# Optimization experiments

Hardware: AMD Instinct MI355X
Metric: run time of the kernel (lower is better)

The kernel has to match this reference:

```python
import jax, jax.numpy as jnp
import numpy as np

T, B, D, H = 2048, 64, 256, 512

def setup_inputs() -> dict:
    key = jax.random.key(0)
    ks = jax.random.split(key, 4)
    s = 1.0 / np.sqrt(D + H)  # nn.Linear default uniform scale approximated with normal*s
    return {
        "x": jax.random.normal(ks[0], (T, B, D), dtype=jnp.float32),
        "h0": jnp.zeros((B, H), dtype=jnp.float32),
        "Wz": jax.random.normal(ks[1], (D + H, H), dtype=jnp.float32) * s,
        "bz": jnp.zeros((H,), dtype=jnp.float32),
        "Wr": jax.random.normal(ks[2], (D + H, H), dtype=jnp.float32) * s,
        "br": jnp.zeros((H,), dtype=jnp.float32),
        "Wh": jax.random.normal(ks[3], (D + H, H), dtype=jnp.float32) * s,
        "bh": jnp.zeros((H,), dtype=jnp.float32),
    }

def reference(x, h0, Wz, bz, Wr, br, Wh, bh):
    """GRU over time: x [T,B,D], h0 [B,H]; returns hidden history [T,B,H]."""
    def step(h, xt):
        xh = jnp.concatenate([xt, h], axis=-1)          # [B, D+H]
        z = jax.nn.sigmoid(xh @ Wz + bz)                # update gate
        r = jax.nn.sigmoid(xh @ Wr + br)                # reset gate
        xrh = jnp.concatenate([xt, r * h], axis=-1)     # [B, D+H]
        h_tilde = jnp.tanh(xrh @ Wh + bh)               # candidate state
        h_new = (1.0 - z) * h + z * h_tilde
        return h_new, h_new
    _, hist = jax.lax.scan(step, h0, x)
    return hist
```

## Files before the change

### kernel.cpp

```cpp
#include <hip/hip_runtime.h>
#include <stdint.h>


#define T_STEPS 2048
#define B_SZ    64
#define D_SZ    256
#define H_SZ    512
#define NGROUP  4
#define NWG     64
#define MB      16
#define CPW     6

typedef __attribute__((ext_vector_type(8))) short  short8;
typedef __attribute__((ext_vector_type(4))) float  f32x4;

__device__ __forceinline__ unsigned short f2bf(float v) {
  uint32_t u = __float_as_uint(v);
  return (unsigned short)((u + 0x7fffu + ((u >> 16) & 1u)) >> 16);
}
__device__ __forceinline__ float bf2f(unsigned short h) {
  return __uint_as_float(((uint32_t)h) << 16);
}
__device__ __forceinline__ void splitf(float v, short& hi, short& lo) {
  unsigned short h = f2bf(v);
  hi = (short)h;
  lo = (short)f2bf(v - bf2f(h));
}
__device__ __forceinline__ uint32_t packf(float v) {
  unsigned short h = f2bf(v);
  unsigned short l = f2bf(v - bf2f(h));
  return ((uint32_t)h << 16) | (uint32_t)l;
}
__device__ __forceinline__ float unpackf(uint32_t p) {
  return __uint_as_float(p & 0xffff0000u) + __uint_as_float(p << 16);
}

__device__ __forceinline__ uint32_t aload32(const uint32_t* p) {
  return __hip_atomic_load(p, __ATOMIC_RELAXED, __HIP_MEMORY_SCOPE_AGENT);
}
__device__ __forceinline__ unsigned long long aload64(const uint32_t* p) {
  return __hip_atomic_load((const unsigned long long*)p, __ATOMIC_RELAXED,
                           __HIP_MEMORY_SCOPE_AGENT);
}
__device__ __forceinline__ void astore32(uint32_t* p, uint32_t v) {
  __hip_atomic_store(p, v, __ATOMIC_RELAXED, __HIP_MEMORY_SCOPE_AGENT);
}

__device__ __forceinline__ void poll_flags(const uint32_t* fl, uint32_t tgt,
                                           int lane, int& cap) {
  int guard = 0;
  for (;;) {
    uint32_t v = aload32(fl + lane);
    if (__all((int)(v >= tgt))) break;
    if (++guard > cap) { cap = 256; break; }
    __builtin_amdgcn_s_sleep(1);
  }
}

__global__ void __launch_bounds__(256, 1)
gru_persistent(const float* __restrict__ x, const float* __restrict__ h0,
               const float* __restrict__ Wz, const float* __restrict__ bz,
               const float* __restrict__ Wr, const float* __restrict__ br,
               const float* __restrict__ Wh, const float* __restrict__ bh,
               float* __restrict__ out,
               uint32_t* zr_flg, uint32_t* h_flg,
               uint32_t* h_pk, uint32_t* rh_pk, uint32_t* z_pk)
{
  __shared__ float partT[16 * 64];
  __shared__ float bias1s[16];
  __shared__ float bias2s[8];

  const int tid  = threadIdx.x;
  const int wv   = tid >> 6;
  const int lane = tid & 63;
  const int blk  = blockIdx.x;
  const int g    = blk >> 6;
  const int wid  = blk & 63;
  const int m0   = g * MB;
  const bool isZ = (wid < 32);
  const int c1   = (wid & 31) * 16;
  const int c2   = wid * 8;
  const float* W1 = isZ ? Wz : Wr;

  const int n     = lane & 15;
  const int kq    = lane >> 4;
  const int bfrag = m0 + n;
  const int m2    = kq * 4 + wv;
  const int n2    = n;
  const int b2    = m0 + m2;

  uint32_t* my_zr = zr_flg + g * 64;
  uint32_t* my_h  = h_flg  + g * 64;

  short8 w1h[CPW], w1l[CPW], w2h[CPW], w2l[CPW];
  #pragma unroll
  for (int i = 0; i < CPW; ++i) {
    const int ch = wv * CPW + i;
    #pragma unroll
    for (int j = 0; j < 8; ++j) {
      const int k = ch * 32 + kq * 8 + j;
      short hi, lo;
      splitf(W1[(size_t)k * H_SZ + c1 + n], hi, lo);
      w1h[i][j] = hi; w1l[i][j] = lo;
      float v = (n < 8) ? Wh[(size_t)k * H_SZ + c2 + n] : 0.f;
      splitf(v, hi, lo);
      w2h[i][j] = hi; w2l[i][j] = lo;
    }
  }
  if (tid < 16)      bias1s[tid] = isZ ? bz[c1 + tid] : br[c1 + tid];
  else if (tid < 24) bias2s[tid - 16] = bh[c2 + (tid - 16)];
  __syncthreads();

  float hreg = (n2 < 8) ? h0[(size_t)b2 * H_SZ + c2 + n2] : 0.f;

  int cap = 1 << 20;

  #pragma unroll 1
  for (int t = 0; t < T_STEPS; ++t) {
    short8 ah[CPW], al[CPW];

    #pragma unroll
    for (int i = 0; i < CPW; ++i) {
      const int ch = wv * CPW + i;
      if (ch < 8) {
        const float* xp = x + ((size_t)t * B_SZ + bfrag) * D_SZ + ch * 32 + kq * 8;
        float4 f0 = *(const float4*)xp;
        float4 f1 = *(const float4*)(xp + 4);
        float f[8] = {f0.x, f0.y, f0.z, f0.w, f1.x, f1.y, f1.z, f1.w};
        #pragma unroll
        for (int j = 0; j < 8; ++j) { short hi, lo; splitf(f[j], hi, lo); ah[i][j] = hi; al[i][j] = lo; }
      }
    }

    if (t > 0) poll_flags(my_h, (uint32_t)t, lane, cap);

    uint32_t hpu = 0; float hp0 = 0.f;
    if (!isZ) {
      if (t > 0) hpu = aload32(h_pk + (size_t)b2 * H_SZ + c1 + n2);
      else       hp0 = h0[(size_t)b2 * H_SZ + c1 + n2];
    }

    #pragma unroll
    for (int i = 0; i < CPW; ++i) {
      const int ch = wv * CPW + i;
      if (ch >= 8) {
        const int kh = ch * 32 - 256 + kq * 8;
        if (t > 0) {
          const uint32_t* hp = h_pk + (size_t)bfrag * H_SZ + kh;
          unsigned long long q0 = aload64(hp),     q1 = aload64(hp + 2);
          unsigned long long q2 = aload64(hp + 4), q3 = aload64(hp + 6);
          uint32_t u[8] = {(uint32_t)q0, (uint32_t)(q0 >> 32), (uint32_t)q1, (uint32_t)(q1 >> 32),
                           (uint32_t)q2, (uint32_t)(q2 >> 32), (uint32_t)q3, (uint32_t)(q3 >> 32)};
          #pragma unroll
          for (int j = 0; j < 8; ++j) { ah[i][j] = (short)(u[j] >> 16); al[i][j] = (short)(u[j] & 0xffffu); }
        } else {
          const float* hp = h0 + (size_t)bfrag * H_SZ + kh;
          float4 f0 = *(const float4*)hp;
          float4 f1 = *(const float4*)(hp + 4);
          float f[8] = {f0.x, f0.y, f0.z, f0.w, f1.x, f1.y, f1.z, f1.w};
          #pragma unroll
          for (int j = 0; j < 8; ++j) { short hi, lo; splitf(f[j], hi, lo); ah[i][j] = hi; al[i][j] = lo; }
        }
      }
    }

    {
      f32x4 acc = {0.f, 0.f, 0.f, 0.f};
      #pragma unroll
      for (int i = 0; i < CPW; ++i) {
        acc = __builtin_amdgcn_mfma_f32_16x16x32_bf16(ah[i], w1h[i], acc, 0, 0, 0);
        acc = __builtin_amdgcn_mfma_f32_16x16x32_bf16(al[i], w1h[i], acc, 0, 0, 0);
        acc = __builtin_amdgcn_mfma_f32_16x16x32_bf16(ah[i], w1l[i], acc, 0, 0, 0);
      }
      #pragma unroll
      for (int r = 0; r < 4; ++r) partT[(wv * 4 + r) * 64 + lane] = acc[r];
    }
    __syncthreads();

    {
      float s = partT[(0 + wv) * 64 + lane] + partT[(4 + wv) * 64 + lane]
              + partT[(8 + wv) * 64 + lane] + partT[(12 + wv) * 64 + lane] + bias1s[n2];
      float sg = 1.f / (1.f + __expf(-s));
      if (isZ) {
        astore32(z_pk + (size_t)b2 * H_SZ + c1 + n2, __float_as_uint(sg));
      } else {
        float hp = (t > 0) ? unpackf(hpu) : hp0;
        astore32(rh_pk + (size_t)b2 * H_SZ + c1 + n2, packf(sg * hp));
      }
    }
    asm volatile("s_waitcnt vmcnt(0)" ::: "memory");
    __syncthreads();
    if (tid == 0) astore32(my_zr + wid, (uint32_t)(t + 1));

    poll_flags(my_zr, (uint32_t)(t + 1), lane, cap);

    uint32_t zu = 0;
    if (n2 < 8) zu = aload32(z_pk + (size_t)b2 * H_SZ + c2 + n2);

    #pragma unroll
    for (int i = 0; i < CPW; ++i) {
      const int ch = wv * CPW + i;
      if (ch >= 8) {
        const int kh = ch * 32 - 256 + kq * 8;
        const uint32_t* rp = rh_pk + (size_t)bfrag * H_SZ + kh;
        unsigned long long q0 = aload64(rp),     q1 = aload64(rp + 2);
        unsigned long long q2 = aload64(rp + 4), q3 = aload64(rp + 6);
        uint32_t u[8] = {(uint32_t)q0, (uint32_t)(q0 >> 32), (uint32_t)q1, (uint32_t)(q1 >> 32),
                         (uint32_t)q2, (uint32_t)(q2 >> 32), (uint32_t)q3, (uint32_t)(q3 >> 32)};
        #pragma unroll
        for (int j = 0; j < 8; ++j) { ah[i][j] = (short)(u[j] >> 16); al[i][j] = (short)(u[j] & 0xffffu); }
      }
    }

    {
      f32x4 acc = {0.f, 0.f, 0.f, 0.f};
      #pragma unroll
      for (int i = 0; i < CPW; ++i) {
        acc = __builtin_amdgcn_mfma_f32_16x16x32_bf16(ah[i], w2h[i], acc, 0, 0, 0);
        acc = __builtin_amdgcn_mfma_f32_16x16x32_bf16(al[i], w2h[i], acc, 0, 0, 0);
        acc = __builtin_amdgcn_mfma_f32_16x16x32_bf16(ah[i], w2l[i], acc, 0, 0, 0);
      }
      #pragma unroll
      for (int r = 0; r < 4; ++r) partT[(wv * 4 + r) * 64 + lane] = acc[r];
    }
    __syncthreads();

    float hn = 0.f; bool live = (n2 < 8);
    if (live) {
      float s = partT[(0 + wv) * 64 + lane] + partT[(4 + wv) * 64 + lane]
              + partT[(8 + wv) * 64 + lane] + partT[(12 + wv) * 64 + lane] + bias2s[n2];
      float e  = __expf(2.f * s);
      float ht = 1.f - 2.f / (e + 1.f);
      float zf = __uint_as_float(zu);
      hn = (1.f - zf) * hreg + zf * ht;
      hreg = hn;
      astore32(h_pk + (size_t)b2 * H_SZ + c2 + n2, packf(hn));
    }
    asm volatile("s_waitcnt vmcnt(0)" ::: "memory");
    __syncthreads();
    if (tid == 0) astore32(my_h + wid, (uint32_t)(t + 1));

    if (live)
      __builtin_nontemporal_store(hn, out + ((size_t)t * B_SZ + b2) * H_SZ + c2 + n2);
  }
}

extern "C" void kernel_launch(void* const* d_in, const int* in_sizes, int n_in,
                              void* d_out, int out_size, void* d_ws, size_t ws_size,
                              hipStream_t stream) {
  const float* x  = (const float*)d_in[0];
  const float* h0 = (const float*)d_in[1];
  const float* Wz = (const float*)d_in[2];
  const float* bz = (const float*)d_in[3];
  const float* Wr = (const float*)d_in[4];
  const float* br = (const float*)d_in[5];
  const float* Wh = (const float*)d_in[6];
  const float* bh = (const float*)d_in[7];
  float* out = (float*)d_out;

  char* ws = (char*)d_ws;
  uint32_t* zr_flg = (uint32_t*)(ws + 0);
  uint32_t* h_flg  = (uint32_t*)(ws + 16384);
  uint32_t* h_pk   = (uint32_t*)(ws + 32768);
  uint32_t* rh_pk  = (uint32_t*)(ws + 163840);
  uint32_t* z_pk   = (uint32_t*)(ws + 294912);

  hipMemsetAsync(d_ws, 0, 32768, stream);
  gru_persistent<<<dim3(NGROUP * NWG), dim3(256), 0, stream>>>(
      x, h0, Wz, bz, Wr, br, Wh, bh, out,
      zr_flg, h_flg, h_pk, rh_pk, z_pk);
}
```

Before: 25.18 ms.

## Replace flag barriers with step-tagged 64-bit data words and a single epoch flag

Each shared value (h, r*h, z) is now stored as a 64-bit word whose upper half holds the step number. Consumers poll the data itself until every tag reaches the target step, which removes the separate flag-store and flag-poll round trips and the vmcnt drains. A single epoch counter per workgroup guards against overwriting h before all peers have read it (write-after-read), and the full __syncthreads calls become s_barrier after an LDS wait. The cost is twice the global traffic per exchanged value, all of it through per-element 64-bit atomic loads, plus a memset of a larger workspace.

```diff
diff --git a/kernel.cpp b/kernel.cpp
--- a/kernel.cpp
+++ b/kernel.cpp
@@ -13,6 +13,7 @@
 
 typedef __attribute__((ext_vector_type(8))) short  short8;
 typedef __attribute__((ext_vector_type(4))) float  f32x4;
+typedef unsigned long long u64;
 
 __device__ __forceinline__ unsigned short f2bf(float v) {
   uint32_t u = __float_as_uint(v);
@@ -38,23 +39,19 @@
 __device__ __forceinline__ uint32_t aload32(const uint32_t* p) {
   return __hip_atomic_load(p, __ATOMIC_RELAXED, __HIP_MEMORY_SCOPE_AGENT);
 }
-__device__ __forceinline__ unsigned long long aload64(const uint32_t* p) {
-  return __hip_atomic_load((const unsigned long long*)p, __ATOMIC_RELAXED,
-                           __HIP_MEMORY_SCOPE_AGENT);
-}
 __device__ __forceinline__ void astore32(uint32_t* p, uint32_t v) {
   __hip_atomic_store(p, v, __ATOMIC_RELAXED, __HIP_MEMORY_SCOPE_AGENT);
 }
-
-__device__ __forceinline__ void poll_flags(const uint32_t* fl, uint32_t tgt,
-                                           int lane, int& cap) {
-  int guard = 0;
-  for (;;) {
-    uint32_t v = aload32(fl + lane);
-    if (__all((int)(v >= tgt))) break;
-    if (++guard > cap) { cap = 256; break; }
-    __builtin_amdgcn_s_sleep(1);
-  }
+__device__ __forceinline__ u64 aload64p(const u64* p) {
+  return __hip_atomic_load(p, __ATOMIC_RELAXED, __HIP_MEMORY_SCOPE_AGENT);
+}
+__device__ __forceinline__ void astore64(u64* p, u64 v) {
+  __hip_atomic_store(p, v, __ATOMIC_RELAXED, __HIP_MEMORY_SCOPE_AGENT);
+}
+
+__device__ __forceinline__ void lds_barrier() {
+  asm volatile("s_waitcnt lgkmcnt(0)" ::: "memory");
+  __builtin_amdgcn_s_barrier();
 }
 
 __global__ void __launch_bounds__(256, 1)
@@ -63,8 +60,8 @@
                const float* __restrict__ Wr, const float* __restrict__ br,
                const float* __restrict__ Wh, const float* __restrict__ bh,
                float* __restrict__ out,
-               uint32_t* zr_flg, uint32_t* h_flg,
-               uint32_t* h_pk, uint32_t* rh_pk, uint32_t* z_pk)
+               uint32_t* epoch,
+               u64* h_pk, u64* rh_pk, u64* z_pk)
 {
   __shared__ float partT[16 * 64];
   __shared__ float bias1s[16];
@@ -89,8 +86,7 @@
   const int n2    = n;
   const int b2    = m0 + m2;
 
-  uint32_t* my_zr = zr_flg + g * 64;
-  uint32_t* my_h  = h_flg  + g * 64;
+  uint32_t* my_ep = epoch + g * 64;
 
   short8 w1h[CPW], w1l[CPW], w2h[CPW], w2l[CPW];
   #pragma unroll
@@ -132,28 +128,43 @@
       }
     }
 
-    if (t > 0) poll_flags(my_h, (uint32_t)t, lane, cap);
-
-    uint32_t hpu = 0; float hp0 = 0.f;
-    if (!isZ) {
-      if (t > 0) hpu = aload32(h_pk + (size_t)b2 * H_SZ + c1 + n2);
-      else       hp0 = h0[(size_t)b2 * H_SZ + c1 + n2];
-    }
-
-    #pragma unroll
-    for (int i = 0; i < CPW; ++i) {
-      const int ch = wv * CPW + i;
-      if (ch >= 8) {
-        const int kh = ch * 32 - 256 + kq * 8;
-        if (t > 0) {
-          const uint32_t* hp = h_pk + (size_t)bfrag * H_SZ + kh;
-          unsigned long long q0 = aload64(hp),     q1 = aload64(hp + 2);
-          unsigned long long q2 = aload64(hp + 4), q3 = aload64(hp + 6);
-          uint32_t u[8] = {(uint32_t)q0, (uint32_t)(q0 >> 32), (uint32_t)q1, (uint32_t)(q1 >> 32),
-                           (uint32_t)q2, (uint32_t)(q2 >> 32), (uint32_t)q3, (uint32_t)(q3 >> 32)};
-          #pragma unroll
-          for (int j = 0; j < 8; ++j) { ah[i][j] = (short)(u[j] >> 16); al[i][j] = (short)(u[j] & 0xffffu); }
-        } else {
+    uint32_t hpv = 0; float hp0 = 0.f;
+    if (t > 0) {
+      const uint32_t tgt = (uint32_t)t;
+      int guard = 0;
+      for (;;) {
+        uint32_t mt = 0xffffffffu;
+        if (!isZ) {
+          u64 q = aload64p(h_pk + (size_t)b2 * H_SZ + c1 + n2);
+          hpv = (uint32_t)q;
+          uint32_t tg = (uint32_t)(q >> 32); mt = tg < mt ? tg : mt;
+        }
+        #pragma unroll
+        for (int i = 0; i < CPW; ++i) {
+          const int ch = wv * CPW + i;
+          if (ch >= 8) {
+            const int kh = ch * 32 - 256 + kq * 8;
+            const u64* hp = h_pk + (size_t)bfrag * H_SZ + kh;
+            #pragma unroll
+            for (int j = 0; j < 8; ++j) {
+              u64 q = aload64p(hp + j);
+              uint32_t tg = (uint32_t)(q >> 32); mt = tg < mt ? tg : mt;
+              uint32_t v = (uint32_t)q;
+              ah[i][j] = (short)(v >> 16); al[i][j] = (short)(v & 0xffffu);
+            }
+          }
+        }
+        if (__all((int)(mt >= tgt))) break;
+        if (++guard > cap) { cap = 256; break; }
+        __builtin_amdgcn_s_sleep(1);
+      }
+    } else {
+      if (!isZ) hp0 = h0[(size_t)b2 * H_SZ + c1 + n2];
+      #pragma unroll
+      for (int i = 0; i < CPW; ++i) {
+        const int ch = wv * CPW + i;
+        if (ch >= 8) {
+          const int kh = ch * 32 - 256 + kq * 8;
           const float* hp = h0 + (size_t)bfrag * H_SZ + kh;
           float4 f0 = *(const float4*)hp;
           float4 f1 = *(const float4*)(hp + 4);
@@ -175,42 +186,57 @@
       #pragma unroll
       for (int r = 0; r < 4; ++r) partT[(wv * 4 + r) * 64 + lane] = acc[r];
     }
-    __syncthreads();
+    lds_barrier();
+
+    if (tid == 0) astore32(my_ep + wid, (uint32_t)(t + 1));
 
     {
       float s = partT[(0 + wv) * 64 + lane] + partT[(4 + wv) * 64 + lane]
               + partT[(8 + wv) * 64 + lane] + partT[(12 + wv) * 64 + lane] + bias1s[n2];
       float sg = 1.f / (1.f + __expf(-s));
+      const u64 tagw = ((u64)(uint32_t)(t + 1)) << 32;
       if (isZ) {
-        astore32(z_pk + (size_t)b2 * H_SZ + c1 + n2, __float_as_uint(sg));
+        astore64(z_pk + (size_t)b2 * H_SZ + c1 + n2, tagw | (u64)__float_as_uint(sg));
       } else {
-        float hp = (t > 0) ? unpackf(hpu) : hp0;
-        astore32(rh_pk + (size_t)b2 * H_SZ + c1 + n2, packf(sg * hp));
-      }
-    }
-    asm volatile("s_waitcnt vmcnt(0)" ::: "memory");
-    __syncthreads();
-    if (tid == 0) astore32(my_zr + wid, (uint32_t)(t + 1));
-
-    poll_flags(my_zr, (uint32_t)(t + 1), lane, cap);
+        float hp = (t > 0) ? unpackf(hpv) : hp0;
+        astore64(rh_pk + (size_t)b2 * H_SZ + c1 + n2, tagw | (u64)packf(sg * hp));
+      }
+    }
+    lds_barrier();
 
     uint32_t zu = 0;
-    if (n2 < 8) zu = aload32(z_pk + (size_t)b2 * H_SZ + c2 + n2);
-
-    #pragma unroll
-    for (int i = 0; i < CPW; ++i) {
-      const int ch = wv * CPW + i;
-      if (ch >= 8) {
-        const int kh = ch * 32 - 256 + kq * 8;
-        const uint32_t* rp = rh_pk + (size_t)bfrag * H_SZ + kh;
-        unsigned long long q0 = aload64(rp),     q1 = aload64(rp + 2);
-        unsigned long long q2 = aload64(rp + 4), q3 = aload64(rp + 6);
-        uint32_t u[8] = {(uint32_t)q0, (uint32_t)(q0 >> 32), (uint32_t)q1, (uint32_t)(q1 >> 32),
-                         (uint32_t)q2, (uint32_t)(q2 >> 32), (uint32_t)q3, (uint32_t)(q3 >> 32)};
+    {
+      const uint32_t tgt2 = (uint32_t)(t + 1);
+      int guard = 0;
+      for (;;) {
+        uint32_t mt = 0xffffffffu;
+        u64 zq = 0;
+        if (n2 < 8) {
+          zq = aload64p(z_pk + (size_t)b2 * H_SZ + c2 + n2);
+          uint32_t tg = (uint32_t)(zq >> 32); mt = tg < mt ? tg : mt;
+        }
         #pragma unroll
-        for (int j = 0; j < 8; ++j) { ah[i][j] = (short)(u[j] >> 16); al[i][j] = (short)(u[j] & 0xffffu); }
-      }
-    }
+        for (int i = 0; i < CPW; ++i) {
+          const int ch = wv * CPW + i;
+          if (ch >= 8) {
+            const int kh = ch * 32 - 256 + kq * 8;
+            const u64* rp = rh_pk + (size_t)bfrag * H_SZ + kh;
+            #pragma unroll
+            for (int j = 0; j < 8; ++j) {
+              u64 q = aload64p(rp + j);
+              uint32_t tg = (uint32_t)(q >> 32); mt = tg < mt ? tg : mt;
+              uint32_t v = (uint32_t)q;
+              ah[i][j] = (short)(v >> 16); al[i][j] = (short)(v & 0xffffu);
+            }
+          }
+        }
+        if (__all((int)(mt >= tgt2))) { zu = (uint32_t)zq; break; }
+        if (++guard > cap) { cap = 256; zu = (uint32_t)zq; break; }
+        __builtin_amdgcn_s_sleep(1);
+      }
+    }
+
+    uint32_t ep = aload32(my_ep + lane);
 
     {
       f32x4 acc = {0.f, 0.f, 0.f, 0.f};
@@ -223,9 +249,9 @@
       #pragma unroll
       for (int r = 0; r < 4; ++r) partT[(wv * 4 + r) * 64 + lane] = acc[r];
     }
-    __syncthreads();
-
-    float hn = 0.f; bool live = (n2 < 8);
+    lds_barrier();
+
+    float hn = 0.f; const bool live = (n2 < 8);
     if (live) {
       float s = partT[(0 + wv) * 64 + lane] + partT[(4 + wv) * 64 + lane]
               + partT[(8 + wv) * 64 + lane] + partT[(12 + wv) * 64 + lane] + bias2s[n2];
@@ -234,14 +260,23 @@
       float zf = __uint_as_float(zu);
       hn = (1.f - zf) * hreg + zf * ht;
       hreg = hn;
-      astore32(h_pk + (size_t)b2 * H_SZ + c2 + n2, packf(hn));
-    }
-    asm volatile("s_waitcnt vmcnt(0)" ::: "memory");
-    __syncthreads();
-    if (tid == 0) astore32(my_h + wid, (uint32_t)(t + 1));
-
-    if (live)
+    }
+
+    {
+      int guard = 0;
+      while (!__all((int)(ep >= (uint32_t)(t + 1)))) {
+        if (++guard > cap) { cap = 256; break; }
+        __builtin_amdgcn_s_sleep(1);
+        ep = aload32(my_ep + lane);
+      }
+    }
+
+    if (live) {
+      const u64 tagw = ((u64)(uint32_t)(t + 1)) << 32;
+      astore64(h_pk + (size_t)b2 * H_SZ + c2 + n2, tagw | (u64)packf(hn));
       __builtin_nontemporal_store(hn, out + ((size_t)t * B_SZ + b2) * H_SZ + c2 + n2);
+    }
+    lds_barrier();
   }
 }
 
@@ -259,14 +294,13 @@
   float* out = (float*)d_out;
 
   char* ws = (char*)d_ws;
-  uint32_t* zr_flg = (uint32_t*)(ws + 0);
-  uint32_t* h_flg  = (uint32_t*)(ws + 16384);
-  uint32_t* h_pk   = (uint32_t*)(ws + 32768);
-  uint32_t* rh_pk  = (uint32_t*)(ws + 163840);
-  uint32_t* z_pk   = (uint32_t*)(ws + 294912);
-
-  hipMemsetAsync(d_ws, 0, 32768, stream);
+  uint32_t* epoch = (uint32_t*)(ws + 0);
+  u64* h_pk  = (u64*)(ws + 4096);
+  u64* rh_pk = (u64*)(ws + 4096 + 262144);
+  u64* z_pk  = (u64*)(ws + 4096 + 524288);
+
+  hipMemsetAsync(d_ws, 0, 4096 + 3 * 262144, stream);
   gru_persistent<<<dim3(NGROUP * NWG), dim3(256), 0, stream>>>(
       x, h0, Wz, bz, Wr, br, Wh, bh, out,
-      zr_flg, h_flg, h_pk, rh_pk, z_pk);
-}
+      epoch, h_pk, rh_pk, z_pk);
+}
```

New measurement: 41.87 ms. 1.66x slower.

## Split workgroups into gate and candidate roles with one-way flag handoffs

Applied to the files above, without the earlier changes.

Workgroups now take a fixed role. Half compute both z and r gates for 16 columns, and the other half compute the candidate state for 16 columns, where each previously used only 8 of its 16 MFMA columns. This replaces the all-to-all barrier within each step with producer-consumer flags (gate→candidate, candidate→gate), and lets the x-projection MFMAs start before waiting on the flags. Per-wave K chunks are rebalanced so each wave handles 2 x-chunks and 4 h-chunks, and the LDS barrier is changed to wait only on lgkmcnt. Gate workgroups now hold twice as many weight registers, which risks register pressure and a longer gate-side critical path.

```diff
diff --git a/kernel.cpp b/kernel.cpp
--- a/kernel.cpp
+++ b/kernel.cpp
@@ -9,10 +9,10 @@
 #define NGROUP  4
 #define NWG     64
 #define MB      16
-#define CPW     6
 
 typedef __attribute__((ext_vector_type(8))) short  short8;
 typedef __attribute__((ext_vector_type(4))) float  f32x4;
+typedef unsigned long long u64;
 
 __device__ __forceinline__ unsigned short f2bf(float v) {
   uint32_t u = __float_as_uint(v);
@@ -38,19 +38,24 @@
 __device__ __forceinline__ uint32_t aload32(const uint32_t* p) {
   return __hip_atomic_load(p, __ATOMIC_RELAXED, __HIP_MEMORY_SCOPE_AGENT);
 }
-__device__ __forceinline__ unsigned long long aload64(const uint32_t* p) {
+__device__ __forceinline__ u64 aload64(const uint32_t* p) {
   return __hip_atomic_load((const unsigned long long*)p, __ATOMIC_RELAXED,
                            __HIP_MEMORY_SCOPE_AGENT);
 }
 __device__ __forceinline__ void astore32(uint32_t* p, uint32_t v) {
   __hip_atomic_store(p, v, __ATOMIC_RELAXED, __HIP_MEMORY_SCOPE_AGENT);
+}
+
+__device__ __forceinline__ void lds_barrier() {
+  asm volatile("s_waitcnt lgkmcnt(0)" ::: "memory");
+  __builtin_amdgcn_s_barrier();
 }
 
 __device__ __forceinline__ void poll_flags(const uint32_t* fl, uint32_t tgt,
                                            int lane, int& cap) {
   int guard = 0;
   for (;;) {
-    uint32_t v = aload32(fl + lane);
+    uint32_t v = aload32(fl + (lane & 31));
     if (__all((int)(v >= tgt))) break;
     if (++guard > cap) { cap = 256; break; }
     __builtin_amdgcn_s_sleep(1);
@@ -58,17 +63,16 @@
 }
 
 __global__ void __launch_bounds__(256, 1)
-gru_persistent(const float* __restrict__ x, const float* __restrict__ h0,
-               const float* __restrict__ Wz, const float* __restrict__ bz,
-               const float* __restrict__ Wr, const float* __restrict__ br,
-               const float* __restrict__ Wh, const float* __restrict__ bh,
-               float* __restrict__ out,
-               uint32_t* zr_flg, uint32_t* h_flg,
-               uint32_t* h_pk, uint32_t* rh_pk, uint32_t* z_pk)
+gru_roles(const float* __restrict__ x, const float* __restrict__ h0,
+          const float* __restrict__ Wz, const float* __restrict__ bz,
+          const float* __restrict__ Wr, const float* __restrict__ br,
+          const float* __restrict__ Wh, const float* __restrict__ bh,
+          float* __restrict__ out,
+          uint32_t* rh_flg, uint32_t* h_flg,
+          uint32_t* h_pk, uint32_t* rh_pk, uint32_t* z_pk)
 {
-  __shared__ float partT[16 * 64];
-  __shared__ float bias1s[16];
-  __shared__ float bias2s[8];
+  __shared__ float partTa[16 * 64];
+  __shared__ float partTb[16 * 64];
 
   const int tid  = threadIdx.x;
   const int wv   = tid >> 6;
@@ -77,10 +81,7 @@
   const int g    = blk >> 6;
   const int wid  = blk & 63;
   const int m0   = g * MB;
-  const bool isZ = (wid < 32);
-  const int c1   = (wid & 31) * 16;
-  const int c2   = wid * 8;
-  const float* W1 = isZ ? Wz : Wr;
+  const bool isGate = (wid < 32);
 
   const int n     = lane & 15;
   const int kq    = lane >> 4;
@@ -89,159 +90,192 @@
   const int n2    = n;
   const int b2    = m0 + m2;
 
-  uint32_t* my_zr = zr_flg + g * 64;
-  uint32_t* my_h  = h_flg  + g * 64;
-
-  short8 w1h[CPW], w1l[CPW], w2h[CPW], w2l[CPW];
+  uint32_t* frh = rh_flg + g * 32;
+  uint32_t* fh  = h_flg  + g * 32;
+
+  int lch[6];
+  lch[0] = 2 * wv; lch[1] = 2 * wv + 1;
   #pragma unroll
-  for (int i = 0; i < CPW; ++i) {
-    const int ch = wv * CPW + i;
+  for (int l = 2; l < 6; ++l) lch[l] = 8 + 4 * wv + (l - 2);
+
+  int cap = 1 << 20;
+
+  if (isGate) {
+    const int c1  = wid * 16;
+    const int col = c1 + n;
+
+    short8 wzh[6], wzl[6], wrh_[6], wrl_[6];
     #pragma unroll
-    for (int j = 0; j < 8; ++j) {
-      const int k = ch * 32 + kq * 8 + j;
-      short hi, lo;
-      splitf(W1[(size_t)k * H_SZ + c1 + n], hi, lo);
-      w1h[i][j] = hi; w1l[i][j] = lo;
-      float v = (n < 8) ? Wh[(size_t)k * H_SZ + c2 + n] : 0.f;
-      splitf(v, hi, lo);
-      w2h[i][j] = hi; w2l[i][j] = lo;
+    for (int l = 0; l < 6; ++l) {
+      #pragma unroll
+      for (int j = 0; j < 8; ++j) {
+        const int k = lch[l] * 32 + kq * 8 + j;
+        short hi, lo;
+        splitf(Wz[(size_t)k * H_SZ + col], hi, lo); wzh[l][j] = hi; wzl[l][j] = lo;
+        splitf(Wr[(size_t)k * H_SZ + col], hi, lo); wrh_[l][j] = hi; wrl_[l][j] = lo;
+      }
     }
-  }
-  if (tid < 16)      bias1s[tid] = isZ ? bz[c1 + tid] : br[c1 + tid];
-  else if (tid < 24) bias2s[tid - 16] = bh[c2 + (tid - 16)];
-  __syncthreads();
-
-  float hreg = (n2 < 8) ? h0[(size_t)b2 * H_SZ + c2 + n2] : 0.f;
-
-  int cap = 1 << 20;
-
-  #pragma unroll 1
-  for (int t = 0; t < T_STEPS; ++t) {
-    short8 ah[CPW], al[CPW];
-
-    #pragma unroll
-    for (int i = 0; i < CPW; ++i) {
-      const int ch = wv * CPW + i;
-      if (ch < 8) {
-        const float* xp = x + ((size_t)t * B_SZ + bfrag) * D_SZ + ch * 32 + kq * 8;
+    const float bzv = bz[col];
+    const float brv = br[col];
+
+    #pragma unroll 1
+    for (int t = 0; t < T_STEPS; ++t) {
+      f32x4 aZ = {0.f, 0.f, 0.f, 0.f};
+      f32x4 aR = {0.f, 0.f, 0.f, 0.f};
+      #pragma unroll
+      for (int l = 0; l < 2; ++l) {
+        const float* xp = x + ((size_t)t * B_SZ + bfrag) * D_SZ + lch[l] * 32 + kq * 8;
         float4 f0 = *(const float4*)xp;
         float4 f1 = *(const float4*)(xp + 4);
         float f[8] = {f0.x, f0.y, f0.z, f0.w, f1.x, f1.y, f1.z, f1.w};
-        #pragma unroll
-        for (int j = 0; j < 8; ++j) { short hi, lo; splitf(f[j], hi, lo); ah[i][j] = hi; al[i][j] = lo; }
-      }
-    }
-
-    if (t > 0) poll_flags(my_h, (uint32_t)t, lane, cap);
-
-    uint32_t hpu = 0; float hp0 = 0.f;
-    if (!isZ) {
-      if (t > 0) hpu = aload32(h_pk + (size_t)b2 * H_SZ + c1 + n2);
-      else       hp0 = h0[(size_t)b2 * H_SZ + c1 + n2];
-    }
-
-    #pragma unroll
-    for (int i = 0; i < CPW; ++i) {
-      const int ch = wv * CPW + i;
-      if (ch >= 8) {
-        const int kh = ch * 32 - 256 + kq * 8;
-        if (t > 0) {
+        short8 xh, xl;
+        #pragma unroll
+        for (int j = 0; j < 8; ++j) { short hi, lo; splitf(f[j], hi, lo); xh[j] = hi; xl[j] = lo; }
+        aZ = __builtin_amdgcn_mfma_f32_16x16x32_bf16(xh, wzh[l], aZ, 0, 0, 0);
+        aZ = __builtin_amdgcn_mfma_f32_16x16x32_bf16(xl, wzh[l], aZ, 0, 0, 0);
+        aZ = __builtin_amdgcn_mfma_f32_16x16x32_bf16(xh, wzl[l], aZ, 0, 0, 0);
+        aR = __builtin_amdgcn_mfma_f32_16x16x32_bf16(xh, wrh_[l], aR, 0, 0, 0);
+        aR = __builtin_amdgcn_mfma_f32_16x16x32_bf16(xl, wrh_[l], aR, 0, 0, 0);
+        aR = __builtin_amdgcn_mfma_f32_16x16x32_bf16(xh, wrl_[l], aR, 0, 0, 0);
+      }
+
+      float hval;
+      if (t > 0) {
+        poll_flags(fh, (uint32_t)t, lane, cap);
+        uint32_t hv = aload32(h_pk + (size_t)b2 * H_SZ + c1 + n2);
+        #pragma unroll
+        for (int l = 2; l < 6; ++l) {
+          const int kh = (lch[l] - 8) * 32 + kq * 8;
           const uint32_t* hp = h_pk + (size_t)bfrag * H_SZ + kh;
-          unsigned long long q0 = aload64(hp),     q1 = aload64(hp + 2);
-          unsigned long long q2 = aload64(hp + 4), q3 = aload64(hp + 6);
+          u64 q0 = aload64(hp),     q1 = aload64(hp + 2);
+          u64 q2 = aload64(hp + 4), q3 = aload64(hp + 6);
           uint32_t u[8] = {(uint32_t)q0, (uint32_t)(q0 >> 32), (uint32_t)q1, (uint32_t)(q1 >> 32),
                            (uint32_t)q2, (uint32_t)(q2 >> 32), (uint32_t)q3, (uint32_t)(q3 >> 32)};
+          short8 hh, hl;
           #pragma unroll
-          for (int j = 0; j < 8; ++j) { ah[i][j] = (short)(u[j] >> 16); al[i][j] = (short)(u[j] & 0xffffu); }
-        } else {
+          for (int j = 0; j < 8; ++j) { hh[j] = (short)(u[j] >> 16); hl[j] = (short)(u[j] & 0xffffu); }
+          aZ = __builtin_amdgcn_mfma_f32_16x16x32_bf16(hh, wzh[l], aZ, 0, 0, 0);
+          aZ = __builtin_amdgcn_mfma_f32_16x16x32_bf16(hl, wzh[l], aZ, 0, 0, 0);
+          aZ = __builtin_amdgcn_mfma_f32_16x16x32_bf16(hh, wzl[l], aZ, 0, 0, 0);
+          aR = __builtin_amdgcn_mfma_f32_16x16x32_bf16(hh, wrh_[l], aR, 0, 0, 0);
+          aR = __builtin_amdgcn_mfma_f32_16x16x32_bf16(hl, wrh_[l], aR, 0, 0, 0);
+          aR = __builtin_amdgcn_mfma_f32_16x16x32_bf16(hh, wrl_[l], aR, 0, 0, 0);
+        }
+        hval = unpackf(hv);
+      } else {
+        hval = h0[(size_t)b2 * H_SZ + c1 + n2];
+        #pragma unroll
+        for (int l = 2; l < 6; ++l) {
+          const int kh = (lch[l] - 8) * 32 + kq * 8;
           const float* hp = h0 + (size_t)bfrag * H_SZ + kh;
           float4 f0 = *(const float4*)hp;
           float4 f1 = *(const float4*)(hp + 4);
           float f[8] = {f0.x, f0.y, f0.z, f0.w, f1.x, f1.y, f1.z, f1.w};
+          short8 hh, hl;
           #pragma unroll
-          for (int j = 0; j < 8; ++j) { short hi, lo; splitf(f[j], hi, lo); ah[i][j] = hi; al[i][j] = lo; }
+          for (int j = 0; j < 8; ++j) { short hi, lo; splitf(f[j], hi, lo); hh[j] = hi; hl[j] = lo; }
+          aZ = __builtin_amdgcn_mfma_f32_16x16x32_bf16(hh, wzh[l], aZ, 0, 0, 0);
+          aZ = __builtin_amdgcn_mfma_f32_16x16x32_bf16(hl, wzh[l], aZ, 0, 0, 0);
+          aZ = __builtin_amdgcn_mfma_f32_16x16x32_bf16(hh, wzl[l], aZ, 0, 0, 0);
+          aR = __builtin_amdgcn_mfma_f32_16x16x32_bf16(hh, wrh_[l], aR, 0, 0, 0);
+          aR = __builtin_amdgcn_mfma_f32_16x16x32_bf16(hl, wrh_[l], aR, 0, 0, 0);
+          aR = __builtin_amdgcn_mfma_f32_16x16x32_bf16(hh, wrl_[l], aR, 0, 0, 0);
         }
       }
+
+      #pragma unroll
+      for (int r = 0; r < 4; ++r) {
+        partTa[(wv * 4 + r) * 64 + lane] = aZ[r];
+        partTb[(wv * 4 + r) * 64 + lane] = aR[r];
+      }
+      lds_barrier();
+      {
+        float sZ = partTa[(0 + wv) * 64 + lane] + partTa[(4 + wv) * 64 + lane]
+                 + partTa[(8 + wv) * 64 + lane] + partTa[(12 + wv) * 64 + lane] + bzv;
+        float sR = partTb[(0 + wv) * 64 + lane] + partTb[(4 + wv) * 64 + lane]
+                 + partTb[(8 + wv) * 64 + lane] + partTb[(12 + wv) * 64 + lane] + brv;
+        float zg = 1.f / (1.f + __expf(-sZ));
+        float rg = 1.f / (1.f + __expf(-sR));
+        astore32(z_pk  + (size_t)b2 * H_SZ + c1 + n2, __float_as_uint(zg));
+        astore32(rh_pk + (size_t)b2 * H_SZ + c1 + n2, packf(rg * hval));
+      }
+      asm volatile("s_waitcnt vmcnt(0)" ::: "memory");
+      lds_barrier();
+      if (tid == 0) astore32(frh + wid, (uint32_t)(t + 1));
     }
-
-    {
+  } else {
+    const int c2  = (wid - 32) * 16;
+    const int col = c2 + n;
+
+    short8 whh_[6], whl_[6];
+    #pragma unroll
+    for (int l = 0; l < 6; ++l) {
+      #pragma unroll
+      for (int j = 0; j < 8; ++j) {
+        const int k = lch[l] * 32 + kq * 8 + j;
+        short hi, lo;
+        splitf(Wh[(size_t)k * H_SZ + col], hi, lo); whh_[l][j] = hi; whl_[l][j] = lo;
+      }
+    }
+    const float bhv = bh[col];
+
+    float hreg = h0[(size_t)b2 * H_SZ + c2 + n2];
+
+    #pragma unroll 1
+    for (int t = 0; t < T_STEPS; ++t) {
       f32x4 acc = {0.f, 0.f, 0.f, 0.f};
       #pragma unroll
-      for (int i = 0; i < CPW; ++i) {
-        acc = __builtin_amdgcn_mfma_f32_16x16x32_bf16(ah[i], w1h[i], acc, 0, 0, 0);
-        acc = __builtin_amdgcn_mfma_f32_16x16x32_bf16(al[i], w1h[i], acc, 0, 0, 0);
-        acc = __builtin_amdgcn_mfma_f32_16x16x32_bf16(ah[i], w1l[i], acc, 0, 0, 0);
-      }
-      #pragma unroll
-      for (int r = 0; r < 4; ++r) partT[(wv * 4 + r) * 64 + lane] = acc[r];
-    }
-    __syncthreads();
-
-    {
-      float s = partT[(0 + wv) * 64 + lane] + partT[(4 + wv) * 64 + lane]
-              + partT[(8 + wv) * 64 + lane] + partT[(12 + wv) * 64 + lane] + bias1s[n2];
-      float sg = 1.f / (1.f + __expf(-s));
-      if (isZ) {
-        astore32(z_pk + (size_t)b2 * H_SZ + c1 + n2, __float_as_uint(sg));
-      } else {
-        float hp = (t > 0) ? unpackf(hpu) : hp0;
-        astore32(rh_pk + (size_t)b2 * H_SZ + c1 + n2, packf(sg * hp));
-      }
-    }
-    asm volatile("s_waitcnt vmcnt(0)" ::: "memory");
-    __syncthreads();
-    if (tid == 0) astore32(my_zr + wid, (uint32_t)(t + 1));
-
-    poll_flags(my_zr, (uint32_t)(t + 1), lane, cap);
-
-    uint32_t zu = 0;
-    if (n2 < 8) zu = aload32(z_pk + (size_t)b2 * H_SZ + c2 + n2);
-
-    #pragma unroll
-    for (int i = 0; i < CPW; ++i) {
-      const int ch = wv * CPW + i;
-      if (ch >= 8) {
-        const int kh = ch * 32 - 256 + kq * 8;
+      for (int l = 0; l < 2; ++l) {
+        const float* xp = x + ((size_t)t * B_SZ + bfrag) * D_SZ + lch[l] * 32 + kq * 8;
+        float4 f0 = *(const float4*)xp;
+        float4 f1 = *(const float4*)(xp + 4);
+        float f[8] = {f0.x, f0.y, f0.z, f0.w, f1.x, f1.y, f1.z, f1.w};
+        short8 xh, xl;
+        #pragma unroll
+        for (int j = 0; j < 8; ++j) { short hi, lo; splitf(f[j], hi, lo); xh[j] = hi; xl[j] = lo; }
+        acc = __builtin_amdgcn_mfma_f32_16x16x32_bf16(xh, whh_[l], acc, 0, 0, 0);
+        acc = __builtin_amdgcn_mfma_f32_16x16x32_bf16(xl, whh_[l], acc, 0, 0, 0);
+        acc = __builtin_amdgcn_mfma_f32_16x16x32_bf16(xh, whl_[l], acc, 0, 0, 0);
+      }
+
+      poll_flags(frh, (uint32_t)(t + 1), lane, cap);
+      uint32_t zu = aload32(z_pk + (size_t)b2 * H_SZ + c2 + n2);
+      #pragma unroll
+      for (int l = 2; l < 6; ++l) {
+        const int kh = (lch[l] - 8) * 32 + kq * 8;
         const uint32_t* rp = rh_pk + (size_t)bfrag * H_SZ + kh;
-        unsigned long long q0 = aload64(rp),     q1 = aload64(rp + 2);
-        unsigned long long q2 = aload64(rp + 4), q3 = aload64(rp + 6);
+        u64 q0 = aload64(rp),     q1 = aload64(rp + 2);
+        u64 q2 = aload64(rp + 4), q3 = aload64(rp + 6);
         uint32_t u[8] = {(uint32_t)q0, (uint32_t)(q0 >> 32), (uint32_t)q1, (uint32_t)(q1 >> 32),
                          (uint32_t)q2, (uint32_t)(q2 >> 32), (uint32_t)q3, (uint32_t)(q3 >> 32)};
-        #pragma unroll
-        for (int j = 0; j < 8; ++j) { ah[i][j] = (short)(u[j] >> 16); al[i][j] = (short)(u[j] & 0xffffu); }
-      }
+        short8 rh8, rl8;
+        #pragma unroll
+        for (int j = 0; j < 8; ++j) { rh8[j] = (short)(u[j] >> 16); rl8[j] = (short)(u[j] & 0xffffu); }
+        acc = __builtin_amdgcn_mfma_f32_16x16x32_bf16(rh8, whh_[l], acc, 0, 0, 0);
+        acc = __builtin_amdgcn_mfma_f32_16x16x32_bf16(rl8, whh_[l], acc, 0, 0, 0);
+        acc = __builtin_amdgcn_mfma_f32_16x16x32_bf16(rh8, whl_[l], acc, 0, 0, 0);
+      }
+
+      #pragma unroll
+      for (int r = 0; r < 4; ++r) partTa[(wv * 4 + r) * 64 + lane] = acc[r];
+      lds_barrier();
+      float hn;
+      {
+        float s = partTa[(0 + wv) * 64 + lane] + partTa[(4 + wv) * 64 + lane]
+                + partTa[(8 + wv) * 64 + lane] + partTa[(12 + wv) * 64 + lane] + bhv;
+        float e  = __expf(2.f * s);
+        float ht = 1.f - 2.f / (e + 1.f);
+        float zf = __uint_as_float(zu);
+        hn = (1.f - zf) * hreg + zf * ht;
+        hreg = hn;
+        astore32(h_pk + (size_t)b2 * H_SZ + c2 + n2, packf(hn));
+      }
+      asm volatile("s_waitcnt vmcnt(0)" ::: "memory");
+      lds_barrier();
+      if (tid == 0) astore32(fh + (wid - 32), (uint32_t)(t + 1));
+
+      __builtin_nontemporal_store(hn, out + ((size_t)t * B_SZ + b2) * H_SZ + c2 + n2);
     }
-
-    {
-      f32x4 acc = {0.f, 0.f, 0.f, 0.f};
-      #pragma unroll
-      for (int i = 0; i < CPW; ++i) {
-        acc = __builtin_amdgcn_mfma_f32_16x16x32_bf16(ah[i], w2h[i], acc, 0, 0, 0);
-        acc = __builtin_amdgcn_mfma_f32_16x16x32_bf16(al[i], w2h[i], acc, 0, 0, 0);
-        acc = __builtin_amdgcn_mfma_f32_16x16x32_bf16(ah[i], w2l[i], acc, 0, 0, 0);
-      }
-      #pragma unroll
-      for (int r = 0; r < 4; ++r) partT[(wv * 4 + r) * 64 + lane] = acc[r];
-    }
-    __syncthreads();
-
-    float hn = 0.f; bool live = (n2 < 8);
-    if (live) {
-      float s = partT[(0 + wv) * 64 + lane] + partT[(4 + wv) * 64 + lane]
-              + partT[(8 + wv) * 64 + lane] + partT[(12 + wv) * 64 + lane] + bias2s[n2];
-      float e  = __expf(2.f * s);
-      float ht = 1.f - 2.f / (e + 1.f);
-      float zf = __uint_as_float(zu);
-      hn = (1.f - zf) * hreg + zf * ht;
-      hreg = hn;
-      astore32(h_pk + (size_t)b2 * H_SZ + c2 + n2, packf(hn));
-    }
-    asm volatile("s_waitcnt vmcnt(0)" ::: "memory");
-    __syncthreads();
-    if (tid == 0) astore32(my_h + wid, (uint32_t)(t + 1));
-
-    if (live)
-      __builtin_nontemporal_store(hn, out + ((size_t)t * B_SZ + b2) * H_SZ + c2 + n2);
   }
 }
 
@@ -259,14 +293,14 @@
   float* out = (float*)d_out;
 
   char* ws = (char*)d_ws;
-  uint32_t* zr_flg = (uint32_t*)(ws + 0);
-  uint32_t* h_flg  = (uint32_t*)(ws + 16384);
-  uint32_t* h_pk   = (uint32_t*)(ws + 32768);
-  uint32_t* rh_pk  = (uint32_t*)(ws + 163840);
-  uint32_t* z_pk   = (uint32_t*)(ws + 294912);
-
-  hipMemsetAsync(d_ws, 0, 32768, stream);
-  gru_persistent<<<dim3(NGROUP * NWG), dim3(256), 0, stream>>>(
+  uint32_t* rh_flg = (uint32_t*)(ws + 0);
+  uint32_t* h_flg  = (uint32_t*)(ws + 2048);
+  uint32_t* h_pk   = (uint32_t*)(ws + 8192);
+  uint32_t* rh_pk  = (uint32_t*)(ws + 8192 + 131072);
+  uint32_t* z_pk   = (uint32_t*)(ws + 8192 + 262144);
+
+  hipMemsetAsync(d_ws, 0, 8192, stream);
+  gru_roles<<<dim3(NGROUP * NWG), dim3(256), 0, stream>>>(
       x, h0, Wz, bz, Wr, br, Wh, bh, out,
-      zr_flg, h_flg, h_pk, rh_pk, z_pk);
-}
+      rh_flg, h_flg, h_pk, rh_pk, z_pk);
+}
```

After: 25.67 ms. No clear change (+1.9%).
